# Kernel optimization log

Hardware: AMD Instinct MI355X
Metric: run time of the kernel (lower is better)

## Reference

```python
import jax, jax.numpy as jnp
import numpy as np

N = 50000
E = 600000
HIDDEN = 128
HEADS = 4
HEAD_DIM = HIDDEN // HEADS
NEG_SLOPE = 0.2
LN_EPS = 1e-5


def setup_inputs() -> dict:
    key = jax.random.key(0)
    ks = jax.random.split(key, 16)
    s = 1.0 / np.sqrt(HIDDEN)
    inp = {
        "h": jax.random.normal(ks[0], (N, HIDDEN), dtype=jnp.float32),
        "src": jax.random.randint(ks[1], (E,), 0, N, dtype=jnp.int32),
        "dst": jax.random.randint(ks[2], (E,), 0, N, dtype=jnp.int32),
        # GATv2 params (share_weights=False, bias=True)
        "W_src": jax.random.normal(ks[3], (HIDDEN, HIDDEN), dtype=jnp.float32) * s,
        "b_src": jnp.zeros((HIDDEN,), dtype=jnp.float32),
        "W_dst": jax.random.normal(ks[4], (HIDDEN, HIDDEN), dtype=jnp.float32) * s,
        "b_dst": jnp.zeros((HIDDEN,), dtype=jnp.float32),
        "attn": jax.random.normal(ks[5], (HEADS, HEAD_DIM), dtype=jnp.float32) * s,
        # FFN params
        "W1": jax.random.normal(ks[6], (HIDDEN, 2 * HIDDEN), dtype=jnp.float32) * s,
        "bf1": jnp.zeros((2 * HIDDEN,), dtype=jnp.float32),
        "W2": jax.random.normal(ks[7], (2 * HIDDEN, HIDDEN), dtype=jnp.float32) * (1.0 / np.sqrt(2 * HIDDEN)),
        "bf2": jnp.zeros((HIDDEN,), dtype=jnp.float32),
        # LayerNorms
        "g1": jnp.ones((HIDDEN,), dtype=jnp.float32),
        "beta1": jnp.zeros((HIDDEN,), dtype=jnp.float32),
        "g2": jnp.ones((HIDDEN,), dtype=jnp.float32),
        "beta2": jnp.zeros((HIDDEN,), dtype=jnp.float32),
    }
    return inp


def _layernorm(x, g, b):
    mu = jnp.mean(x, axis=-1, keepdims=True)
    var = jnp.mean(jnp.square(x - mu), axis=-1, keepdims=True)
    return (x - mu) * jax.lax.rsqrt(var + LN_EPS) * g + b


def reference(h, src, dst, W_src, b_src, W_dst, b_dst, attn,
              W1, bf1, W2, bf2, g1, beta1, g2, beta2):
    # --- GATv2 attention (eval mode, dropouts are identity) ---
    fs = (h @ W_src + b_src).reshape(N, HEADS, HEAD_DIM)   # [N,H,D]
    fd = (h @ W_dst + b_dst).reshape(N, HEADS, HEAD_DIM)
    e = jax.nn.leaky_relu(fs[src] + fd[dst], NEG_SLOPE)    # [E,H,D]
    logits = jnp.einsum('ehd,hd->eh', e, attn)             # [E,H]
    # edge softmax over incoming edges of each dst node
    m = jax.ops.segment_max(logits, dst, num_segments=N)   # [N,H]
    m = jnp.where(jnp.isfinite(m), m, 0.0)                 # guard zero-in-degree
    a = jnp.exp(logits - m[dst])                           # [E,H]
    denom = jax.ops.segment_sum(a, dst, num_segments=N)    # [N,H]
    denom = jnp.where(denom == 0.0, 1.0, denom)
    alpha = a / denom[dst]                                 # [E,H]
    msg = fs[src] * alpha[:, :, None]                      # [E,H,D]
    rst = jax.ops.segment_sum(msg, dst, num_segments=N)    # [N,H,D]
    h_attn = rst.reshape(N, HIDDEN)
    # --- residual + LN, FFN + residual + LN ---
    h1 = _layernorm(h + h_attn, g1, beta1)
    ffn = jax.nn.gelu(h1 @ W1 + bf1, approximate=False) @ W2 + bf2
    out = _layernorm(h1 + ffn, g2, beta2)
    return out
```

## Files before the change

kernel.cpp:

```cpp
#include <hip/hip_runtime.h>
#include <math.h>

#define N_NODES 50000
#define N_EDGES 600000
#define HID 128
#define FFN_HID 256
#define NEG_SLOPE 0.2f
#define LN_EPS 1e-5f
#define BKT 64
#define CSTR 16

typedef unsigned short u16;
typedef unsigned int u32;
typedef __attribute__((ext_vector_type(8))) short short8;
typedef __attribute__((ext_vector_type(4))) float floatx4;

__device__ __forceinline__ u16 f2bf(float x) {
    unsigned int u = __float_as_uint(x);
    unsigned int r = u + 0x7FFFu + ((u >> 16) & 1u);
    return (u16)(r >> 16);
}
__device__ __forceinline__ float bflo(u32 u) { return __uint_as_float(u << 16); }
__device__ __forceinline__ float bfhi(u32 u) { return __uint_as_float(u & 0xffff0000u); }
__device__ __forceinline__ u32 packbf(float lo, float hi) {
    return (u32)f2bf(lo) | ((u32)f2bf(hi) << 16);
}
__device__ __forceinline__ float bf2f(u16 v) { return __uint_as_float(((u32)v) << 16); }
__device__ __forceinline__ float gelu_fast(float v) {
    float u = 1.5957691216057308f * fmaf(0.044715f * v * v, v, v);
    return v / (1.0f + __expf(-u));
}


__global__ __launch_bounds__(256) void scatter_gemm(
    const int* __restrict__ src, const int* __restrict__ dst,
    int* __restrict__ cursor, u16* __restrict__ ebkt,
    const float* __restrict__ h,
    const float* __restrict__ Wsrc, const float* __restrict__ Wdst,
    const float* __restrict__ bsrc, const float* __restrict__ bdst,
    u16* __restrict__ fsb, u16* __restrict__ fdb)
{
    int bid = blockIdx.x;
    bool isGemm = (bid < 1536) && ((bid % 3) != 2);
    if (!isGemm) {
        int sid = (bid < 1536) ? (bid / 3) : (512 + bid - 1536);
        int t4 = sid * 256 + threadIdx.x;
        if (t4 < N_EDGES / 4) {
            uint4 d4 = *(const uint4*)&dst[t4 * 4];
            uint4 s4 = *(const uint4*)&src[t4 * 4];
            int slot0 = atomicAdd(&cursor[(int)d4.x * CSTR], 1);
            int slot1 = atomicAdd(&cursor[(int)d4.y * CSTR], 1);
            int slot2 = atomicAdd(&cursor[(int)d4.z * CSTR], 1);
            int slot3 = atomicAdd(&cursor[(int)d4.w * CSTR], 1);
            if (slot0 < BKT) ebkt[(size_t)d4.x * BKT + slot0] = (u16)s4.x;
            if (slot1 < BKT) ebkt[(size_t)d4.y * BKT + slot1] = (u16)s4.y;
            if (slot2 < BKT) ebkt[(size_t)d4.z * BKT + slot2] = (u16)s4.z;
            if (slot3 < BKT) ebkt[(size_t)d4.w * BKT + slot3] = (u16)s4.w;
        }
        return;
    }
    int gid = (bid / 3) * 2 + (bid % 3);
    int tid = threadIdx.x, wave = tid >> 6, lane = tid & 63;
    int lrow = lane & 15, lq = lane >> 4;
    short8 bfrag[4][4];
    float bias[4];
    #pragma unroll
    for (int nt = 0; nt < 4; nt++) {
        int cg = wave * 64 + nt * 16 + lrow;
        const float* Wp = (cg < HID) ? (Wsrc + cg) : (Wdst + cg - HID);
        bias[nt] = (cg < HID) ? bsrc[cg] : bdst[cg - HID];
        #pragma unroll
        for (int ks = 0; ks < 4; ks++) {
            short8 b;
            #pragma unroll
            for (int j = 0; j < 8; j++)
                b[j] = (short)f2bf(Wp[(size_t)(ks * 32 + lq * 8 + j) * HID]);
            bfrag[nt][ks] = b;
        }
    }
    for (int mb = gid; mb < N_NODES / 16; mb += 1024) {
        int m0 = mb * 16;
        const float* hrow = h + (size_t)(m0 + lrow) * HID;
        floatx4 acc[4];
        #pragma unroll
        for (int nt = 0; nt < 4; nt++) acc[nt] = {0.f, 0.f, 0.f, 0.f};
        #pragma unroll
        for (int ks = 0; ks < 4; ks++) {
            float4 va = *(const float4*)(hrow + ks * 32 + lq * 8);
            float4 vb = *(const float4*)(hrow + ks * 32 + lq * 8 + 4);
            short8 a;
            a[0] = (short)f2bf(va.x); a[1] = (short)f2bf(va.y);
            a[2] = (short)f2bf(va.z); a[3] = (short)f2bf(va.w);
            a[4] = (short)f2bf(vb.x); a[5] = (short)f2bf(vb.y);
            a[6] = (short)f2bf(vb.z); a[7] = (short)f2bf(vb.w);
            #pragma unroll
            for (int nt = 0; nt < 4; nt++)
                acc[nt] = __builtin_amdgcn_mfma_f32_16x16x32_bf16(a, bfrag[nt][ks], acc[nt], 0, 0, 0);
        }
        #pragma unroll
        for (int nt = 0; nt < 4; nt++) {
            int cg = wave * 64 + nt * 16 + lrow;
            u16* outp = (cg < HID) ? fsb : fdb;
            int c = cg & (HID - 1);
            #pragma unroll
            for (int r = 0; r < 4; r++) {
                int row = m0 + lq * 4 + r;
                outp[(size_t)row * HID + c] = f2bf(acc[nt][r] + bias[nt]);
            }
        }
    }
}


__global__ __launch_bounds__(256) void aggregate_kernel(
    const u16* __restrict__ fsb, const u16* __restrict__ fdb,
    const float* __restrict__ h, const float* __restrict__ attn,
    const int* __restrict__ cursor, const u16* __restrict__ ebkt,
    const float* __restrict__ g1, const float* __restrict__ beta1,
    u16* __restrict__ h1b)
{
    int wave = threadIdx.x >> 6, lane = threadIdx.x & 63;
    int node = blockIdx.x * 4 + wave;
    if (node >= N_NODES) return;
    int grp = lane >> 4, fl = lane & 15;
    int f = fl * 8;

    uint4 ud = *(const uint4*)&fdb[(size_t)node * HID + f];
    float fdv[8] = { bflo(ud.x), bfhi(ud.x), bflo(ud.y), bfhi(ud.y),
                     bflo(ud.z), bfhi(ud.z), bflo(ud.w), bfhi(ud.w) };
    float4 aA = *(const float4*)&attn[f];
    float4 aB = *(const float4*)&attn[f + 4];
    float c1[8] = { 0.6f * aA.x, 0.6f * aA.y, 0.6f * aA.z, 0.6f * aA.w,
                    0.6f * aB.x, 0.6f * aB.y, 0.6f * aB.z, 0.6f * aB.w };
    float c2[8] = { 0.4f * aA.x, 0.4f * aA.y, 0.4f * aA.z, 0.4f * aA.w,
                    0.4f * aB.x, 0.4f * aB.y, 0.4f * aB.z, 0.4f * aB.w };

    int cnt = cursor[node * CSTR]; cnt = cnt < BKT ? cnt : BKT;
    const u16* brow = ebkt + (size_t)node * BKT;
    float acc[8] = {0.f, 0.f, 0.f, 0.f, 0.f, 0.f, 0.f, 0.f};
    float lsum = 0.f;

    auto loadrow = [&](int e) -> uint4 {
        int s = (int)brow[e];
        return *(const uint4*)&fsb[(size_t)s * HID + f];
    };
    auto compute = [&](uint4 u) {
        float x[8] = { bflo(u.x), bfhi(u.x), bflo(u.y), bfhi(u.y),
                       bflo(u.z), bfhi(u.z), bflo(u.w), bfhi(u.w) };
        float p = 0.f;
        #pragma unroll
        for (int i = 0; i < 8; i++) {
            float ei = x[i] + fdv[i];
            p = fmaf(c1[i], ei, p);
            p = fmaf(c2[i], fabsf(ei), p);
        }
        p += __shfl_xor(p, 1); p += __shfl_xor(p, 2);
        float w = __expf(p);
        lsum += w;
        #pragma unroll
        for (int i = 0; i < 8; i++) acc[i] = fmaf(w, x[i], acc[i]);
    };

    {
        int e = grp;
        uint4 bufA, bufB;
        bool vA = (e < cnt), vB = (e + 4 < cnt);
        if (vA) bufA = loadrow(e);
        if (vB) bufB = loadrow(e + 4);
        while (vA) {
            int en = e + 8;
            uint4 bufC; bool vC = (en < cnt);
            if (vC) bufC = loadrow(en);
            compute(bufA);
            bufA = bufB; vA = vB;
            bufB = bufC; vB = vC;
            e += 4;
        }
    }

    #pragma unroll
    for (int i = 0; i < 8; i++) {
        acc[i] += __shfl_xor(acc[i], 16);
        acc[i] += __shfl_xor(acc[i], 32);
    }
    lsum += __shfl_xor(lsum, 16); lsum += __shfl_xor(lsum, 32);

    float inv = (lsum > 0.f) ? (1.0f / lsum) : 0.f;
    float4 h0 = *(const float4*)&h[(size_t)node * HID + f];
    float4 h1v = *(const float4*)&h[(size_t)node * HID + f + 4];
    float hx[8] = { h0.x, h0.y, h0.z, h0.w, h1v.x, h1v.y, h1v.z, h1v.w };
    float o[8], s1 = 0.f, s2 = 0.f;
    #pragma unroll
    for (int i = 0; i < 8; i++) {
        o[i] = hx[i] + acc[i] * inv;
        s1 += o[i]; s2 += o[i] * o[i];
    }
    s1 += __shfl_xor(s1, 1); s2 += __shfl_xor(s2, 1);
    s1 += __shfl_xor(s1, 2); s2 += __shfl_xor(s2, 2);
    s1 += __shfl_xor(s1, 4); s2 += __shfl_xor(s2, 4);
    s1 += __shfl_xor(s1, 8); s2 += __shfl_xor(s2, 8);
    float mu = s1 * (1.0f / HID);
    float var = s2 * (1.0f / HID) - mu * mu;
    float rs = rsqrtf(var + LN_EPS);
    if (grp == 0) {
        float4 gA = *(const float4*)&g1[f], gB = *(const float4*)&g1[f + 4];
        float4 bA = *(const float4*)&beta1[f], bB = *(const float4*)&beta1[f + 4];
        float q0 = (o[0] - mu) * rs * gA.x + bA.x, q1 = (o[1] - mu) * rs * gA.y + bA.y;
        float q2 = (o[2] - mu) * rs * gA.z + bA.z, q3 = (o[3] - mu) * rs * gA.w + bA.w;
        float q4 = (o[4] - mu) * rs * gB.x + bB.x, q5 = (o[5] - mu) * rs * gB.y + bB.y;
        float q6 = (o[6] - mu) * rs * gB.z + bB.z, q7 = (o[7] - mu) * rs * gB.w + bB.w;
        uint4 ob;
        ob.x = packbf(q0, q1); ob.y = packbf(q2, q3);
        ob.z = packbf(q4, q5); ob.w = packbf(q6, q7);
        *(uint4*)&h1b[(size_t)node * HID + f] = ob;
    }
}


#define TS_PAD 8

__global__ __launch_bounds__(256) void ffn_fused(
    const u16* __restrict__ h1b,
    const float* __restrict__ W1, const float* __restrict__ W2,
    const float* __restrict__ bf1, const float* __restrict__ bf2,
    const float* __restrict__ g2, const float* __restrict__ beta2,
    float* __restrict__ out)
{
    __shared__ u16 ts[16][FFN_HID + TS_PAD];
    __shared__ float xs[16][HID];
    int tid = threadIdx.x, wave = tid >> 6, lane = tid & 63;
    int lrow = lane & 15, lq = lane >> 4;

    short8 b1f[4][4];
    #pragma unroll
    for (int nt = 0; nt < 4; nt++) {
        int cg = wave * 64 + nt * 16 + lrow;
        #pragma unroll
        for (int ks = 0; ks < 4; ks++) {
            short8 b;
            #pragma unroll
            for (int j = 0; j < 8; j++)
                b[j] = (short)f2bf(W1[(size_t)(ks * 32 + lq * 8 + j) * FFN_HID + cg]);
            b1f[nt][ks] = b;
        }
    }
    short8 b2f[2][8];
    #pragma unroll
    for (int nt = 0; nt < 2; nt++) {
        int cg = wave * 32 + nt * 16 + lrow;
        #pragma unroll
        for (int ks = 0; ks < 8; ks++) {
            short8 b;
            #pragma unroll
            for (int j = 0; j < 8; j++)
                b[j] = (short)f2bf(W2[(size_t)(ks * 32 + lq * 8 + j) * HID + cg]);
            b2f[nt][ks] = b;
        }
    }
    float bias1[4];
    #pragma unroll
    for (int nt = 0; nt < 4; nt++) bias1[nt] = bf1[wave * 64 + nt * 16 + lrow];
    float bias2[2];
    #pragma unroll
    for (int nt = 0; nt < 2; nt++) bias2[nt] = bf2[wave * 32 + nt * 16 + lrow];

    for (int mb = blockIdx.x; mb < N_NODES / 16; mb += gridDim.x) {
        int m0 = mb * 16;
        floatx4 acc1[4];
        #pragma unroll
        for (int nt = 0; nt < 4; nt++) acc1[nt] = {0.f, 0.f, 0.f, 0.f};
        #pragma unroll
        for (int ks = 0; ks < 4; ks++) {
            short8 a = *(const short8*)(h1b + (size_t)(m0 + lrow) * HID + ks * 32 + lq * 8);
            #pragma unroll
            for (int nt = 0; nt < 4; nt++)
                acc1[nt] = __builtin_amdgcn_mfma_f32_16x16x32_bf16(a, b1f[nt][ks], acc1[nt], 0, 0, 0);
        }
        #pragma unroll
        for (int nt = 0; nt < 4; nt++) {
            int cg = wave * 64 + nt * 16 + lrow;
            #pragma unroll
            for (int r = 0; r < 4; r++) {
                float v = acc1[nt][r] + bias1[nt];
                ts[lq * 4 + r][cg] = f2bf(gelu_fast(v));
            }
        }
        __syncthreads();
        floatx4 acc2[2];
        #pragma unroll
        for (int nt = 0; nt < 2; nt++) acc2[nt] = {0.f, 0.f, 0.f, 0.f};
        #pragma unroll
        for (int ks = 0; ks < 8; ks++) {
            short8 a = *(const short8*)&ts[lrow][ks * 32 + lq * 8];
            #pragma unroll
            for (int nt = 0; nt < 2; nt++)
                acc2[nt] = __builtin_amdgcn_mfma_f32_16x16x32_bf16(a, b2f[nt][ks], acc2[nt], 0, 0, 0);
        }
        #pragma unroll
        for (int nt = 0; nt < 2; nt++) {
            int cg = wave * 32 + nt * 16 + lrow;
            #pragma unroll
            for (int r = 0; r < 4; r++) {
                int row = m0 + lq * 4 + r;
                float resid = bf2f(h1b[(size_t)row * HID + cg]);
                xs[lq * 4 + r][cg] = acc2[nt][r] + bias2[nt] + resid;
            }
        }
        __syncthreads();
        int row = tid >> 4, c0 = (tid & 15) * 8;
        float v[8];
        float s1 = 0.f, s2 = 0.f;
        #pragma unroll
        for (int i = 0; i < 8; i++) { v[i] = xs[row][c0 + i]; s1 += v[i]; s2 += v[i] * v[i]; }
        s1 += __shfl_xor(s1, 1); s2 += __shfl_xor(s2, 1);
        s1 += __shfl_xor(s1, 2); s2 += __shfl_xor(s2, 2);
        s1 += __shfl_xor(s1, 4); s2 += __shfl_xor(s2, 4);
        s1 += __shfl_xor(s1, 8); s2 += __shfl_xor(s2, 8);
        float mu = s1 * (1.0f / HID);
        float var = s2 * (1.0f / HID) - mu * mu;
        float rs = rsqrtf(var + LN_EPS);
        float o[8];
        #pragma unroll
        for (int i = 0; i < 8; i++) o[i] = (v[i] - mu) * rs * g2[c0 + i] + beta2[c0 + i];
        float* op = out + (size_t)(m0 + row) * HID + c0;
        *(float4*)(op)     = make_float4(o[0], o[1], o[2], o[3]);
        *(float4*)(op + 4) = make_float4(o[4], o[5], o[6], o[7]);
        __syncthreads();
    }
}


extern "C" void kernel_launch(void* const* d_in, const int* in_sizes, int n_in,
                              void* d_out, int out_size, void* d_ws, size_t ws_size,
                              hipStream_t stream)
{
    const float* h    = (const float*)d_in[0];
    const int*   src  = (const int*)d_in[1];
    const int*   dst  = (const int*)d_in[2];
    const float* Wsrc = (const float*)d_in[3];
    const float* bsrc = (const float*)d_in[4];
    const float* Wdst = (const float*)d_in[5];
    const float* bdst = (const float*)d_in[6];
    const float* attn = (const float*)d_in[7];
    const float* W1   = (const float*)d_in[8];
    const float* bf1  = (const float*)d_in[9];
    const float* W2   = (const float*)d_in[10];
    const float* bf2  = (const float*)d_in[11];
    const float* g1   = (const float*)d_in[12];
    const float* beta1= (const float*)d_in[13];
    const float* g2   = (const float*)d_in[14];
    const float* beta2= (const float*)d_in[15];
    float* out = (float*)d_out;

    u16* fsb = (u16*)d_ws;
    u16* fdb = fsb + (size_t)N_NODES * HID;
    u16* h1b = fdb + (size_t)N_NODES * HID;
    int* cursor = (int*)(h1b + (size_t)N_NODES * HID);
    u16* ebkt   = (u16*)(cursor + (size_t)N_NODES * CSTR);

    hipMemsetAsync(cursor, 0, (size_t)N_NODES * CSTR * sizeof(int), stream);
    scatter_gemm<<<1610, 256, 0, stream>>>(src, dst, cursor, ebkt,
                                           h, Wsrc, Wdst, bsrc, bdst, fsb, fdb);
    aggregate_kernel<<<(N_NODES + 3) / 4, 256, 0, stream>>>(fsb, fdb, h, attn, cursor, ebkt, g1, beta1, h1b);
    ffn_fused<<<640, 256, 0, stream>>>(h1b, W1, W2, bf1, bf2, g2, beta2, out);
}
```

Measured before the change: 221.0 us.

## Fuse edge aggregation with FFN into one persistent kernel using LDS staging

Merges the aggregation and FFN kernels into one persistent kernel of 512-thread blocks. Each block aggregates 16 nodes per tile (8 waves, 2 passes), keeps the LN1 output in shared memory, then runs both FFN GEMMs with weights held in registers across 8 waves. This removes the h1b global round trip and one kernel launch. The cost is extra syncs per tile, and the gather phase now runs only 625 blocks under a 4-blocks-per-CU bound, which may reduce the latency hiding available for the irregular gathers.

```diff
diff --git a/kernel.cpp b/kernel.cpp
--- a/kernel.cpp
+++ b/kernel.cpp
@@ -112,22 +112,25 @@
 }
 
 
-__global__ __launch_bounds__(256) void aggregate_kernel(
+#define FF_TILES (N_NODES / 16)
+
+__global__ __launch_bounds__(512, 4) void agg_ffn(
     const u16* __restrict__ fsb, const u16* __restrict__ fdb,
     const float* __restrict__ h, const float* __restrict__ attn,
     const int* __restrict__ cursor, const u16* __restrict__ ebkt,
     const float* __restrict__ g1, const float* __restrict__ beta1,
-    u16* __restrict__ h1b)
+    const float* __restrict__ W1, const float* __restrict__ W2,
+    const float* __restrict__ bf1, const float* __restrict__ bf2,
+    const float* __restrict__ g2, const float* __restrict__ beta2,
+    float* __restrict__ out)
 {
-    int wave = threadIdx.x >> 6, lane = threadIdx.x & 63;
-    int node = blockIdx.x * 4 + wave;
-    if (node >= N_NODES) return;
-    int grp = lane >> 4, fl = lane & 15;
-    int f = fl * 8;
-
-    uint4 ud = *(const uint4*)&fdb[(size_t)node * HID + f];
-    float fdv[8] = { bflo(ud.x), bfhi(ud.x), bflo(ud.y), bfhi(ud.y),
-                     bflo(ud.z), bfhi(ud.z), bflo(ud.w), bfhi(ud.w) };
+    __shared__ u16 h1s[16][HID + 8];
+    __shared__ u16 ts[16][FFN_HID + 8];
+    __shared__ float xs[16][HID + 4];
+    int tid = threadIdx.x, w = tid >> 6, lane = tid & 63;
+    int lrow = lane & 15, lq = lane >> 4;
+    int grp = lq, f = lrow * 8;
+
     float4 aA = *(const float4*)&attn[f];
     float4 aB = *(const float4*)&attn[f + 4];
     float c1[8] = { 0.6f * aA.x, 0.6f * aA.y, 0.6f * aA.z, 0.6f * aA.w,
@@ -135,106 +138,12 @@
     float c2[8] = { 0.4f * aA.x, 0.4f * aA.y, 0.4f * aA.z, 0.4f * aA.w,
                     0.4f * aB.x, 0.4f * aB.y, 0.4f * aB.z, 0.4f * aB.w };
 
-    int cnt = cursor[node * CSTR]; cnt = cnt < BKT ? cnt : BKT;
-    const u16* brow = ebkt + (size_t)node * BKT;
-    float acc[8] = {0.f, 0.f, 0.f, 0.f, 0.f, 0.f, 0.f, 0.f};
-    float lsum = 0.f;
-
-    auto loadrow = [&](int e) -> uint4 {
-        int s = (int)brow[e];
-        return *(const uint4*)&fsb[(size_t)s * HID + f];
-    };
-    auto compute = [&](uint4 u) {
-        float x[8] = { bflo(u.x), bfhi(u.x), bflo(u.y), bfhi(u.y),
-                       bflo(u.z), bfhi(u.z), bflo(u.w), bfhi(u.w) };
-        float p = 0.f;
-        #pragma unroll
-        for (int i = 0; i < 8; i++) {
-            float ei = x[i] + fdv[i];
-            p = fmaf(c1[i], ei, p);
-            p = fmaf(c2[i], fabsf(ei), p);
-        }
-        p += __shfl_xor(p, 1); p += __shfl_xor(p, 2);
-        float w = __expf(p);
-        lsum += w;
-        #pragma unroll
-        for (int i = 0; i < 8; i++) acc[i] = fmaf(w, x[i], acc[i]);
-    };
-
-    {
-        int e = grp;
-        uint4 bufA, bufB;
-        bool vA = (e < cnt), vB = (e + 4 < cnt);
-        if (vA) bufA = loadrow(e);
-        if (vB) bufB = loadrow(e + 4);
-        while (vA) {
-            int en = e + 8;
-            uint4 bufC; bool vC = (en < cnt);
-            if (vC) bufC = loadrow(en);
-            compute(bufA);
-            bufA = bufB; vA = vB;
-            bufB = bufC; vB = vC;
-            e += 4;
-        }
-    }
-
+    short8 b1f[2][4];
+    float bias1[2];
     #pragma unroll
-    for (int i = 0; i < 8; i++) {
-        acc[i] += __shfl_xor(acc[i], 16);
-        acc[i] += __shfl_xor(acc[i], 32);
-    }
-    lsum += __shfl_xor(lsum, 16); lsum += __shfl_xor(lsum, 32);
-
-    float inv = (lsum > 0.f) ? (1.0f / lsum) : 0.f;
-    float4 h0 = *(const float4*)&h[(size_t)node * HID + f];
-    float4 h1v = *(const float4*)&h[(size_t)node * HID + f + 4];
-    float hx[8] = { h0.x, h0.y, h0.z, h0.w, h1v.x, h1v.y, h1v.z, h1v.w };
-    float o[8], s1 = 0.f, s2 = 0.f;
-    #pragma unroll
-    for (int i = 0; i < 8; i++) {
-        o[i] = hx[i] + acc[i] * inv;
-        s1 += o[i]; s2 += o[i] * o[i];
-    }
-    s1 += __shfl_xor(s1, 1); s2 += __shfl_xor(s2, 1);
-    s1 += __shfl_xor(s1, 2); s2 += __shfl_xor(s2, 2);
-    s1 += __shfl_xor(s1, 4); s2 += __shfl_xor(s2, 4);
-    s1 += __shfl_xor(s1, 8); s2 += __shfl_xor(s2, 8);
-    float mu = s1 * (1.0f / HID);
-    float var = s2 * (1.0f / HID) - mu * mu;
-    float rs = rsqrtf(var + LN_EPS);
-    if (grp == 0) {
-        float4 gA = *(const float4*)&g1[f], gB = *(const float4*)&g1[f + 4];
-        float4 bA = *(const float4*)&beta1[f], bB = *(const float4*)&beta1[f + 4];
-        float q0 = (o[0] - mu) * rs * gA.x + bA.x, q1 = (o[1] - mu) * rs * gA.y + bA.y;
-        float q2 = (o[2] - mu) * rs * gA.z + bA.z, q3 = (o[3] - mu) * rs * gA.w + bA.w;
-        float q4 = (o[4] - mu) * rs * gB.x + bB.x, q5 = (o[5] - mu) * rs * gB.y + bB.y;
-        float q6 = (o[6] - mu) * rs * gB.z + bB.z, q7 = (o[7] - mu) * rs * gB.w + bB.w;
-        uint4 ob;
-        ob.x = packbf(q0, q1); ob.y = packbf(q2, q3);
-        ob.z = packbf(q4, q5); ob.w = packbf(q6, q7);
-        *(uint4*)&h1b[(size_t)node * HID + f] = ob;
-    }
-}
-
-
-#define TS_PAD 8
-
-__global__ __launch_bounds__(256) void ffn_fused(
-    const u16* __restrict__ h1b,
-    const float* __restrict__ W1, const float* __restrict__ W2,
-    const float* __restrict__ bf1, const float* __restrict__ bf2,
-    const float* __restrict__ g2, const float* __restrict__ beta2,
-    float* __restrict__ out)
-{
-    __shared__ u16 ts[16][FFN_HID + TS_PAD];
-    __shared__ float xs[16][HID];
-    int tid = threadIdx.x, wave = tid >> 6, lane = tid & 63;
-    int lrow = lane & 15, lq = lane >> 4;
-
-    short8 b1f[4][4];
-    #pragma unroll
-    for (int nt = 0; nt < 4; nt++) {
-        int cg = wave * 64 + nt * 16 + lrow;
+    for (int nt = 0; nt < 2; nt++) {
+        int cg = w * 32 + nt * 16 + lrow;
+        bias1[nt] = bf1[cg];
         #pragma unroll
         for (int ks = 0; ks < 4; ks++) {
             short8 b;
@@ -244,41 +153,120 @@
             b1f[nt][ks] = b;
         }
     }
-    short8 b2f[2][8];
+    short8 b2f[8];
+    int cg2 = w * 16 + lrow;
+    float bias2 = bf2[cg2];
     #pragma unroll
-    for (int nt = 0; nt < 2; nt++) {
-        int cg = wave * 32 + nt * 16 + lrow;
-        #pragma unroll
-        for (int ks = 0; ks < 8; ks++) {
-            short8 b;
-            #pragma unroll
-            for (int j = 0; j < 8; j++)
-                b[j] = (short)f2bf(W2[(size_t)(ks * 32 + lq * 8 + j) * HID + cg]);
-            b2f[nt][ks] = b;
-        }
-    }
-    float bias1[4];
-    #pragma unroll
-    for (int nt = 0; nt < 4; nt++) bias1[nt] = bf1[wave * 64 + nt * 16 + lrow];
-    float bias2[2];
-    #pragma unroll
-    for (int nt = 0; nt < 2; nt++) bias2[nt] = bf2[wave * 32 + nt * 16 + lrow];
-
-    for (int mb = blockIdx.x; mb < N_NODES / 16; mb += gridDim.x) {
+    for (int ks = 0; ks < 8; ks++) {
+        short8 b;
+        #pragma unroll
+        for (int j = 0; j < 8; j++)
+            b[j] = (short)f2bf(W2[(size_t)(ks * 32 + lq * 8 + j) * HID + cg2]);
+        b2f[ks] = b;
+    }
+
+    for (int mb = blockIdx.x; mb < FF_TILES; mb += gridDim.x) {
         int m0 = mb * 16;
-        floatx4 acc1[4];
-        #pragma unroll
-        for (int nt = 0; nt < 4; nt++) acc1[nt] = {0.f, 0.f, 0.f, 0.f};
+        #pragma unroll
+        for (int pass = 0; pass < 2; pass++) {
+            int rl = pass * 8 + w;
+            int node = m0 + rl;
+            uint4 ud = *(const uint4*)&fdb[(size_t)node * HID + f];
+            float fdv[8] = { bflo(ud.x), bfhi(ud.x), bflo(ud.y), bfhi(ud.y),
+                             bflo(ud.z), bfhi(ud.z), bflo(ud.w), bfhi(ud.w) };
+            int cnt = cursor[node * CSTR]; cnt = cnt < BKT ? cnt : BKT;
+            const u16* brow = ebkt + (size_t)node * BKT;
+            float acc[8] = {0.f, 0.f, 0.f, 0.f, 0.f, 0.f, 0.f, 0.f};
+            float lsum = 0.f;
+
+            auto loadrow = [&](int e) -> uint4 {
+                int s = (int)brow[e];
+                return *(const uint4*)&fsb[(size_t)s * HID + f];
+            };
+            auto compute = [&](uint4 u) {
+                float x[8] = { bflo(u.x), bfhi(u.x), bflo(u.y), bfhi(u.y),
+                               bflo(u.z), bfhi(u.z), bflo(u.w), bfhi(u.w) };
+                float p = 0.f;
+                #pragma unroll
+                for (int i = 0; i < 8; i++) {
+                    float ei = x[i] + fdv[i];
+                    p = fmaf(c1[i], ei, p);
+                    p = fmaf(c2[i], fabsf(ei), p);
+                }
+                p += __shfl_xor(p, 1); p += __shfl_xor(p, 2);
+                float wgt = __expf(p);
+                lsum += wgt;
+                #pragma unroll
+                for (int i = 0; i < 8; i++) acc[i] = fmaf(wgt, x[i], acc[i]);
+            };
+
+            {
+                int e = grp;
+                uint4 bufA, bufB;
+                bool vA = (e < cnt), vB = (e + 4 < cnt);
+                if (vA) bufA = loadrow(e);
+                if (vB) bufB = loadrow(e + 4);
+                while (vA) {
+                    int en = e + 8;
+                    uint4 bufC; bool vC = (en < cnt);
+                    if (vC) bufC = loadrow(en);
+                    compute(bufA);
+                    bufA = bufB; vA = vB;
+                    bufB = bufC; vB = vC;
+                    e += 4;
+                }
+            }
+            #pragma unroll
+            for (int i = 0; i < 8; i++) {
+                acc[i] += __shfl_xor(acc[i], 16);
+                acc[i] += __shfl_xor(acc[i], 32);
+            }
+            lsum += __shfl_xor(lsum, 16); lsum += __shfl_xor(lsum, 32);
+
+            float inv = (lsum > 0.f) ? (1.0f / lsum) : 0.f;
+            float4 h0 = *(const float4*)&h[(size_t)node * HID + f];
+            float4 h1v = *(const float4*)&h[(size_t)node * HID + f + 4];
+            float hx[8] = { h0.x, h0.y, h0.z, h0.w, h1v.x, h1v.y, h1v.z, h1v.w };
+            float o[8], s1 = 0.f, s2 = 0.f;
+            #pragma unroll
+            for (int i = 0; i < 8; i++) {
+                o[i] = hx[i] + acc[i] * inv;
+                s1 += o[i]; s2 += o[i] * o[i];
+            }
+            s1 += __shfl_xor(s1, 1); s2 += __shfl_xor(s2, 1);
+            s1 += __shfl_xor(s1, 2); s2 += __shfl_xor(s2, 2);
+            s1 += __shfl_xor(s1, 4); s2 += __shfl_xor(s2, 4);
+            s1 += __shfl_xor(s1, 8); s2 += __shfl_xor(s2, 8);
+            float mu = s1 * (1.0f / HID);
+            float var = s2 * (1.0f / HID) - mu * mu;
+            float rs = rsqrtf(var + LN_EPS);
+            if (grp == 0) {
+                float4 gA = *(const float4*)&g1[f], gB = *(const float4*)&g1[f + 4];
+                float4 bA = *(const float4*)&beta1[f], bB = *(const float4*)&beta1[f + 4];
+                float q0 = (o[0] - mu) * rs * gA.x + bA.x, q1 = (o[1] - mu) * rs * gA.y + bA.y;
+                float q2 = (o[2] - mu) * rs * gA.z + bA.z, q3 = (o[3] - mu) * rs * gA.w + bA.w;
+                float q4 = (o[4] - mu) * rs * gB.x + bB.x, q5 = (o[5] - mu) * rs * gB.y + bB.y;
+                float q6 = (o[6] - mu) * rs * gB.z + bB.z, q7 = (o[7] - mu) * rs * gB.w + bB.w;
+                uint4 ob;
+                ob.x = packbf(q0, q1); ob.y = packbf(q2, q3);
+                ob.z = packbf(q4, q5); ob.w = packbf(q6, q7);
+                *(uint4*)&h1s[rl][f] = ob;
+            }
+        }
+        __syncthreads();
+        floatx4 acc1[2];
+        #pragma unroll
+        for (int nt = 0; nt < 2; nt++) acc1[nt] = {0.f, 0.f, 0.f, 0.f};
         #pragma unroll
         for (int ks = 0; ks < 4; ks++) {
-            short8 a = *(const short8*)(h1b + (size_t)(m0 + lrow) * HID + ks * 32 + lq * 8);
-            #pragma unroll
-            for (int nt = 0; nt < 4; nt++)
+            short8 a = *(const short8*)&h1s[lrow][ks * 32 + lq * 8];
+            #pragma unroll
+            for (int nt = 0; nt < 2; nt++)
                 acc1[nt] = __builtin_amdgcn_mfma_f32_16x16x32_bf16(a, b1f[nt][ks], acc1[nt], 0, 0, 0);
         }
         #pragma unroll
-        for (int nt = 0; nt < 4; nt++) {
-            int cg = wave * 64 + nt * 16 + lrow;
+        for (int nt = 0; nt < 2; nt++) {
+            int cg = w * 32 + nt * 16 + lrow;
             #pragma unroll
             for (int r = 0; r < 4; r++) {
                 float v = acc1[nt][r] + bias1[nt];
@@ -286,45 +274,40 @@
             }
         }
         __syncthreads();
-        floatx4 acc2[2];
-        #pragma unroll
-        for (int nt = 0; nt < 2; nt++) acc2[nt] = {0.f, 0.f, 0.f, 0.f};
+        floatx4 acc2 = {0.f, 0.f, 0.f, 0.f};
         #pragma unroll
         for (int ks = 0; ks < 8; ks++) {
             short8 a = *(const short8*)&ts[lrow][ks * 32 + lq * 8];
-            #pragma unroll
-            for (int nt = 0; nt < 2; nt++)
-                acc2[nt] = __builtin_amdgcn_mfma_f32_16x16x32_bf16(a, b2f[nt][ks], acc2[nt], 0, 0, 0);
-        }
-        #pragma unroll
-        for (int nt = 0; nt < 2; nt++) {
-            int cg = wave * 32 + nt * 16 + lrow;
-            #pragma unroll
-            for (int r = 0; r < 4; r++) {
-                int row = m0 + lq * 4 + r;
-                float resid = bf2f(h1b[(size_t)row * HID + cg]);
-                xs[lq * 4 + r][cg] = acc2[nt][r] + bias2[nt] + resid;
-            }
+            acc2 = __builtin_amdgcn_mfma_f32_16x16x32_bf16(a, b2f[ks], acc2, 0, 0, 0);
+        }
+        #pragma unroll
+        for (int r = 0; r < 4; r++) {
+            int row = lq * 4 + r;
+            xs[row][cg2] = acc2[r] + bias2 + bf2f(h1s[row][cg2]);
         }
         __syncthreads();
-        int row = tid >> 4, c0 = (tid & 15) * 8;
-        float v[8];
-        float s1 = 0.f, s2 = 0.f;
-        #pragma unroll
-        for (int i = 0; i < 8; i++) { v[i] = xs[row][c0 + i]; s1 += v[i]; s2 += v[i] * v[i]; }
-        s1 += __shfl_xor(s1, 1); s2 += __shfl_xor(s2, 1);
-        s1 += __shfl_xor(s1, 2); s2 += __shfl_xor(s2, 2);
-        s1 += __shfl_xor(s1, 4); s2 += __shfl_xor(s2, 4);
-        s1 += __shfl_xor(s1, 8); s2 += __shfl_xor(s2, 8);
-        float mu = s1 * (1.0f / HID);
-        float var = s2 * (1.0f / HID) - mu * mu;
-        float rs = rsqrtf(var + LN_EPS);
-        float o[8];
-        #pragma unroll
-        for (int i = 0; i < 8; i++) o[i] = (v[i] - mu) * rs * g2[c0 + i] + beta2[c0 + i];
-        float* op = out + (size_t)(m0 + row) * HID + c0;
-        *(float4*)(op)     = make_float4(o[0], o[1], o[2], o[3]);
-        *(float4*)(op + 4) = make_float4(o[4], o[5], o[6], o[7]);
+        {
+            int row = tid >> 5, c0 = (tid & 31) * 4;
+            float4 v = *(const float4*)&xs[row][c0];
+            float s1 = v.x + v.y + v.z + v.w;
+            float s2 = v.x * v.x + v.y * v.y + v.z * v.z + v.w * v.w;
+            s1 += __shfl_xor(s1, 1); s2 += __shfl_xor(s2, 1);
+            s1 += __shfl_xor(s1, 2); s2 += __shfl_xor(s2, 2);
+            s1 += __shfl_xor(s1, 4); s2 += __shfl_xor(s2, 4);
+            s1 += __shfl_xor(s1, 8); s2 += __shfl_xor(s2, 8);
+            s1 += __shfl_xor(s1, 16); s2 += __shfl_xor(s2, 16);
+            float mu = s1 * (1.0f / HID);
+            float var = s2 * (1.0f / HID) - mu * mu;
+            float rstd = rsqrtf(var + LN_EPS);
+            float4 gv = *(const float4*)&g2[c0];
+            float4 bv = *(const float4*)&beta2[c0];
+            float4 ov;
+            ov.x = (v.x - mu) * rstd * gv.x + bv.x;
+            ov.y = (v.y - mu) * rstd * gv.y + bv.y;
+            ov.z = (v.z - mu) * rstd * gv.z + bv.z;
+            ov.w = (v.w - mu) * rstd * gv.w + bv.w;
+            *(float4*)&out[(size_t)(m0 + row) * HID + c0] = ov;
+        }
         __syncthreads();
     }
 }
@@ -354,13 +337,12 @@
 
     u16* fsb = (u16*)d_ws;
     u16* fdb = fsb + (size_t)N_NODES * HID;
-    u16* h1b = fdb + (size_t)N_NODES * HID;
-    int* cursor = (int*)(h1b + (size_t)N_NODES * HID);
+    int* cursor = (int*)(fdb + (size_t)N_NODES * HID);
     u16* ebkt   = (u16*)(cursor + (size_t)N_NODES * CSTR);
 
     hipMemsetAsync(cursor, 0, (size_t)N_NODES * CSTR * sizeof(int), stream);
     scatter_gemm<<<1610, 256, 0, stream>>>(src, dst, cursor, ebkt,
                                            h, Wsrc, Wdst, bsrc, bdst, fsb, fdb);
-    aggregate_kernel<<<(N_NODES + 3) / 4, 256, 0, stream>>>(fsb, fdb, h, attn, cursor, ebkt, g1, beta1, h1b);
-    ffn_fused<<<640, 256, 0, stream>>>(h1b, W1, W2, bf1, bf2, g2, beta2, out);
-}
+    agg_ffn<<<625, 512, 0, stream>>>(fsb, fdb, h, attn, cursor, ebkt,
+                                     g1, beta1, W1, W2, bf1, bf2, g2, beta2, out);
+}
```

Result: slower. 321.8 us (+45.6%).
